# Optimization experiments

Hardware: AMD Instinct MI355X
Metric: run time of the kernel (lower is better)

Reference implementation:

```python
import jax, jax.numpy as jnp
import numpy as np


def setup_inputs() -> dict:
    key = jax.random.key(0)
    kx, kw = jax.random.split(key)
    x = jax.random.normal(kx, (2, 64, 16, 128, 128), dtype=jnp.float32)
    # Conv3d(in=2, out=1, kernel=7, padding=3, bias=False) weight, OIDHW layout
    w = jax.random.normal(kw, (1, 2, 7, 7, 7), dtype=jnp.float32) * (1.0 / np.sqrt(2 * 7 * 7 * 7))
    return {"x": x, "w": w}


def reference(x, w):
    # x: (B, C, T, H, W); w: (O=1, I=2, 7, 7, 7)
    max_out = jnp.max(x, axis=1, keepdims=True)   # (B,1,T,H,W)
    avg_out = jnp.mean(x, axis=1, keepdims=True)  # (B,1,T,H,W)
    concat = jnp.concatenate([max_out, avg_out], axis=1)  # (B,2,T,H,W)
    conv = jax.lax.conv_general_dilated(
        concat, w,
        window_strides=(1, 1, 1),
        padding=[(3, 3), (3, 3), (3, 3)],
        dimension_numbers=("NCDHW", "OIDHW", "NCDHW"),
    )  # (B,1,T,H,W)
    attn = jax.nn.sigmoid(conv)
    return attn * x
```

## Files before the change

### kernel.cpp

```cpp
#include <hip/hip_runtime.h>
#include <math.h>


#define NP (2 * 16 * 128 * 128)
#define SMH 14
#define SMW 134
#define SMSTRIDE 136
#define SMCH (SMH * SMSTRIDE)

typedef float vfloat4 __attribute__((ext_vector_type(4)));
typedef float vfloat2 __attribute__((ext_vector_type(2)));

__global__ __launch_bounds__(256) void pool_kernel(const float* __restrict__ x,
                                                   float* __restrict__ pmax,
                                                   float* __restrict__ pavg) {
    int j = blockIdx.x * 256 + threadIdx.x;
    int b = j >> 16;
    int rest = j & 65535;
    const float4* x4 = (const float4*)x;
    int base = (b << 22) | rest;

    float4 v = x4[base];
    float4 vmax = v;
    float4 vsum = v;
#pragma unroll 8
    for (int c = 1; c < 64; ++c) {
        float4 u = x4[base + (c << 16)];
        vmax.x = fmaxf(vmax.x, u.x);
        vmax.y = fmaxf(vmax.y, u.y);
        vmax.z = fmaxf(vmax.z, u.z);
        vmax.w = fmaxf(vmax.w, u.w);
        vsum.x += u.x; vsum.y += u.y; vsum.z += u.z; vsum.w += u.w;
    }
    const float s = 1.0f / 64.0f;
    float4 vavg; vavg.x = vsum.x * s; vavg.y = vsum.y * s; vavg.z = vsum.z * s; vavg.w = vsum.w * s;
    ((float4*)pmax)[j] = vmax;
    ((float4*)pavg)[j] = vavg;
}

__global__ __launch_bounds__(256) void conv_mul_kernel(const float* __restrict__ pooled,
                                                       const float* __restrict__ wgt,
                                                       const float* __restrict__ x,
                                                       float* __restrict__ out) {
    __shared__ __align__(16) float sm[2 * SMCH];

    int bid = blockIdx.x;
    int strip = bid & 15;
    int t = (bid >> 4) & 15;
    int b = bid >> 8;
    int th0 = strip << 3;

    int tid = threadIdx.x;
    int ty = tid >> 5;
    int tx = tid & 31;

    int base4 = (b << 22) + (t << 12) + ((th0 + ty) << 5) + tx;
    int cs = bid & 63;
    const vfloat4* x4 = (const vfloat4*)x;
    vfloat4* o4 = (vfloat4*)out;

    vfloat4 pre[16];
#pragma unroll
    for (int k = 0; k < 16; ++k)
        pre[k] = x4[base4 + (((cs + k) & 63) << 16)];

    float acc0 = 0.f, acc1 = 0.f, acc2 = 0.f, acc3 = 0.f;

    for (int dz = 0; dz < 7; ++dz) {
        int tsrc = t + dz - 3;
        if (tsrc < 0 || tsrc >= 16) continue;

        __syncthreads();
#pragma unroll
        for (int r = 0; r < 15; ++r) {
            int i = tid + (r << 8);
            int ch = i / SMCH;
            int rem = i - ch * SMCH;
            int y = rem / SMSTRIDE;
            int xx = rem - y * SMSTRIDE;
            int gh = th0 + y - 3;
            int gw = xx - 3;
            float val = 0.f;
            if (i < 2 * SMCH && xx < SMW && (unsigned)gh < 128u && (unsigned)gw < 128u)
                val = pooled[ch * NP + (((b << 4) + tsrc) << 14) + (gh << 7) + gw];
            if (i < 2 * SMCH)
                sm[i] = val;
        }
        __syncthreads();

        const float* wdz = wgt + dz * 49;
#pragma unroll
        for (int ch = 0; ch < 2; ++ch) {
#pragma unroll
            for (int dy = 0; dy < 7; ++dy) {
                const float* rp = &sm[ch * SMCH + (ty + dy) * SMSTRIDE + (tx << 2)];
                vfloat4 r0 = *(const vfloat4*)rp;
                vfloat4 r1 = *(const vfloat4*)(rp + 4);
                vfloat2 r2 = *(const vfloat2*)(rp + 8);
                float row[10] = {r0.x, r0.y, r0.z, r0.w,
                                 r1.x, r1.y, r1.z, r1.w,
                                 r2.x, r2.y};
                const float* wr = wdz + ch * 343 + dy * 7;
#pragma unroll
                for (int dx = 0; dx < 7; ++dx) {
                    float wv = wr[dx];
                    acc0 = fmaf(wv, row[dx + 0], acc0);
                    acc1 = fmaf(wv, row[dx + 1], acc1);
                    acc2 = fmaf(wv, row[dx + 2], acc2);
                    acc3 = fmaf(wv, row[dx + 3], acc3);
                }
            }
        }
    }

    vfloat4 av;
    av.x = 1.f / (1.f + __expf(-acc0));
    av.y = 1.f / (1.f + __expf(-acc1));
    av.z = 1.f / (1.f + __expf(-acc2));
    av.w = 1.f / (1.f + __expf(-acc3));

#pragma unroll
    for (int k = 0; k < 16; ++k) {
        int idx = base4 + (((cs + k) & 63) << 16);
        o4[idx] = pre[k] * av;
    }
    for (int cch = 1; cch < 4; ++cch) {
        vfloat4 buf[16];
#pragma unroll
        for (int k = 0; k < 16; ++k)
            buf[k] = x4[base4 + (((cs + (cch << 4) + k) & 63) << 16)];
        __builtin_amdgcn_sched_barrier(0);
#pragma unroll
        for (int k = 0; k < 16; ++k) {
            int idx = base4 + (((cs + (cch << 4) + k) & 63) << 16);
            o4[idx] = buf[k] * av;
        }
    }
}

extern "C" void kernel_launch(void* const* d_in, const int* in_sizes, int n_in,
                              void* d_out, int out_size, void* d_ws, size_t ws_size,
                              hipStream_t stream) {
    const float* x = (const float*)d_in[0];
    const float* w = (const float*)d_in[1];
    float* out = (float*)d_out;
    float* ws = (float*)d_ws;

    float* pmax = ws;
    float* pavg = ws + NP;

    pool_kernel<<<NP / 4 / 256, 256, 0, stream>>>(x, pmax, pavg);
    conv_mul_kernel<<<2 * 16 * 16, 256, 0, stream>>>(pmax, w, x, out);
}
```

Baseline: 271.5 us.

## Split conv and multiply into separate kernels with wide-grid nontemporal multiply

Splits the fused conv+multiply kernel into a conv kernel that writes the sigmoid attention map to workspace, and a separate multiply kernel. The multiply kernel runs a 4096-block grid, each thread covering 8 channels, and uses nontemporal stores. Before, only 512 blocks each streamed all 64 channels, which limited memory parallelism. The cost is one extra launch and a small attention-map round trip through memory.

```diff
diff --git a/kernel.cpp b/kernel.cpp
--- a/kernel.cpp
+++ b/kernel.cpp
@@ -38,10 +38,9 @@
     ((float4*)pavg)[j] = vavg;
 }
 
-__global__ __launch_bounds__(256) void conv_mul_kernel(const float* __restrict__ pooled,
-                                                       const float* __restrict__ wgt,
-                                                       const float* __restrict__ x,
-                                                       float* __restrict__ out) {
+__global__ __launch_bounds__(256) void conv_kernel(const float* __restrict__ pooled,
+                                                   const float* __restrict__ wgt,
+                                                   float* __restrict__ attn) {
     __shared__ __align__(16) float sm[2 * SMCH];
 
     int bid = blockIdx.x;
@@ -53,16 +52,6 @@
     int tid = threadIdx.x;
     int ty = tid >> 5;
     int tx = tid & 31;
-
-    int base4 = (b << 22) + (t << 12) + ((th0 + ty) << 5) + tx;
-    int cs = bid & 63;
-    const vfloat4* x4 = (const vfloat4*)x;
-    vfloat4* o4 = (vfloat4*)out;
-
-    vfloat4 pre[16];
-#pragma unroll
-    for (int k = 0; k < 16; ++k)
-        pre[k] = x4[base4 + (((cs + k) & 63) << 16)];
 
     float acc0 = 0.f, acc1 = 0.f, acc2 = 0.f, acc3 = 0.f;
 
@@ -119,23 +108,33 @@
     av.z = 1.f / (1.f + __expf(-acc2));
     av.w = 1.f / (1.f + __expf(-acc3));
 
+    int aidx = (((b << 4) + t) << 12) + ((th0 + ty) << 5) + tx;
+    ((vfloat4*)attn)[aidx] = av;
+}
+
+__global__ __launch_bounds__(256) void mul_kernel(const float* __restrict__ x,
+                                                  const float* __restrict__ attn,
+                                                  float* __restrict__ out) {
+    int g = blockIdx.x * 256 + threadIdx.x;
+    int s = g & 65535;
+    int cg = g >> 16;
+    int b = cg >> 3;
+    int c0 = (cg & 7) << 3;
+
+    const vfloat4* x4 = (const vfloat4*)x;
+    const vfloat4* a4 = (const vfloat4*)attn;
+    vfloat4* o4 = (vfloat4*)out;
+
+    vfloat4 a = a4[(b << 16) | s];
+    int base = (b << 22) | (c0 << 16) | s;
+
+    vfloat4 buf[8];
 #pragma unroll
-    for (int k = 0; k < 16; ++k) {
-        int idx = base4 + (((cs + k) & 63) << 16);
-        o4[idx] = pre[k] * av;
-    }
-    for (int cch = 1; cch < 4; ++cch) {
-        vfloat4 buf[16];
+    for (int k = 0; k < 8; ++k)
+        buf[k] = x4[base + (k << 16)];
 #pragma unroll
-        for (int k = 0; k < 16; ++k)
-            buf[k] = x4[base4 + (((cs + (cch << 4) + k) & 63) << 16)];
-        __builtin_amdgcn_sched_barrier(0);
-#pragma unroll
-        for (int k = 0; k < 16; ++k) {
-            int idx = base4 + (((cs + (cch << 4) + k) & 63) << 16);
-            o4[idx] = buf[k] * av;
-        }
-    }
+    for (int k = 0; k < 8; ++k)
+        __builtin_nontemporal_store(buf[k] * a, &o4[base + (k << 16)]);
 }
 
 extern "C" void kernel_launch(void* const* d_in, const int* in_sizes, int n_in,
@@ -148,7 +147,9 @@
 
     float* pmax = ws;
     float* pavg = ws + NP;
+    float* attn = ws + 2 * NP;
 
     pool_kernel<<<NP / 4 / 256, 256, 0, stream>>>(x, pmax, pavg);
-    conv_mul_kernel<<<2 * 16 * 16, 256, 0, stream>>>(pmax, w, x, out);
+    conv_kernel<<<2 * 16 * 16, 256, 0, stream>>>(pmax, w, attn);
+    mul_kernel<<<4096, 256, 0, stream>>>(x, attn, out);
 }
```

New measurement: 274.4 us. About the same (+1.1%).
